# Kernel optimization log

Measured on AMD Instinct MI355X. Metric: run time of the kernel, lower is better.

## Reference

```python
import jax, jax.numpy as jnp
import numpy as np

B, N = 1, 512
CS, CZ, H, CH, PQ, PV = 384, 128, 12, 16, 4, 8
INF, EPS = 1e5, 1e-8
SOFTPLUS_INV_1 = 0.541324854612918


def _init_linear(key, fan_in, fan_out):
    kw, kb = jax.random.split(key)
    std = float(1.0 / np.sqrt(fan_in))
    w = jax.random.normal(kw, (fan_in, fan_out), dtype=jnp.float32) * std
    b = jnp.zeros((fan_out,), dtype=jnp.float32)
    return w, b


def setup_inputs() -> dict:
    key = jax.random.key(0)
    ks = jax.random.split(key, 12)
    s = jax.random.normal(ks[0], (B, N, CS), dtype=jnp.float32)
    z = jax.random.normal(ks[1], (B, N, N, CZ), dtype=jnp.float32) * 0.1
    # proper rotation matrices via QR of random Gaussians
    rot, _ = jnp.linalg.qr(jax.random.normal(ks[2], (B, N, 3, 3), dtype=jnp.float32))
    trans = jax.random.normal(ks[3], (B, N, 3), dtype=jnp.float32) * 10.0
    mask = jnp.ones((B, N), dtype=jnp.float32)
    w_q, b_q = _init_linear(ks[4], CS, H * CH)
    w_kv, b_kv = _init_linear(ks[5], CS, 2 * H * CH)
    w_qp, b_qp = _init_linear(ks[6], CS, H * PQ * 3)
    w_kvp, b_kvp = _init_linear(ks[7], CS, H * (PQ + PV) * 3)
    w_b, b_b = _init_linear(ks[8], CZ, H)
    head_weights = jnp.full((H,), SOFTPLUS_INV_1, dtype=jnp.float32)
    concat_dim = H * (CZ + CH + PV * 4)
    # 'final' init -> zeros
    w_out = jnp.zeros((concat_dim, CS), dtype=jnp.float32)
    b_out = jnp.zeros((CS,), dtype=jnp.float32)
    return dict(s=s, z=z, rot=rot, trans=trans, mask=mask,
                w_q=w_q, b_q=b_q, w_kv=w_kv, b_kv=b_kv,
                w_qp=w_qp, b_qp=b_qp, w_kvp=w_kvp, b_kvp=b_kvp,
                w_b=w_b, b_b=b_b, head_weights=head_weights,
                w_out=w_out, b_out=b_out)


def reference(s, z, rot, trans, mask,
              w_q, b_q, w_kv, b_kv, w_qp, b_qp, w_kvp, b_kvp,
              w_b, b_b, head_weights, w_out, b_out):
    # scalar q/k/v: [B,N,H,CH]
    q = (s @ w_q + b_q).reshape(B, N, H, CH)
    kv = (s @ w_kv + b_kv).reshape(B, N, H, 2 * CH)
    k, v = kv[..., :CH], kv[..., CH:]

    def make_points(w, b, P):
        p = s @ w + b                                   # [B,N,3*H*P] (x|y|z chunks)
        p = jnp.moveaxis(p.reshape(B, N, 3, H * P), -2, -1)  # [B,N,H*P,3]
        p = jnp.einsum('bnij,bnpj->bnpi', rot, p) + trans[:, :, None]  # global frame
        return p.reshape(B, N, H, P, 3)

    q_pts = make_points(w_qp, b_qp, PQ)                 # [B,N,H,PQ,3]
    kv_pts = make_points(w_kvp, b_kvp, PQ + PV)
    k_pts, v_pts = kv_pts[..., :PQ, :], kv_pts[..., PQ:, :]

    # scalar QK attention + pair bias
    a = jnp.einsum('bqhc,bkhc->bhqk', q, k) * float(np.sqrt(1.0 / (3 * CH)))
    b_bias = z @ w_b + b_b                              # [B,N,N,H]
    a = a + float(np.sqrt(1.0 / 3.0)) * jnp.moveaxis(b_bias, -1, -3)

    # squared point-distance attention
    d = q_pts[:, :, None] - k_pts[:, None]              # [B,N,N,H,PQ,3]
    pt_att = jnp.sum(d * d, axis=-1)                    # [B,N,N,H,PQ]
    hw = jax.nn.softplus(head_weights) * float(np.sqrt(1.0 / (3 * (PQ * 9.0 / 2))))
    pt_att = -0.5 * jnp.sum(pt_att * hw[None, None, None, :, None], axis=-1)  # [B,N,N,H]
    a = a + jnp.moveaxis(pt_att, -1, -3)                # [B,H,N,N]

    sq_mask = (mask[:, :, None] * mask[:, None, :] - 1.0) * INF
    a = jax.nn.softmax(a + sq_mask[:, None], axis=-1)   # [B,H,N,N]

    # standard value path
    o = jnp.einsum('bhqk,bkhc->bqhc', a, v).reshape(B, N, H * CH)
    # point value path, rotated back to local frame
    o_pt = jnp.einsum('bhqk,bkhpc->bqhpc', a, v_pts)    # [B,N,H,PV,3]
    o_pt = jnp.einsum('bnji,bnhpj->bnhpi', rot, o_pt - trans[:, :, None, None])
    o_pt_norm = jnp.sqrt(jnp.sum(o_pt ** 2, axis=-1) + EPS).reshape(B, N, H * PV)
    o_pt = o_pt.reshape(B, N, H * PV, 3)
    # pair-weighted path
    o_pair = jnp.einsum('bhqk,bqkc->bqhc', a, z).reshape(B, N, H * CZ)

    o_cat = jnp.concatenate(
        [o, o_pt[..., 0], o_pt[..., 1], o_pt[..., 2], o_pt_norm, o_pair], axis=-1)
    return o_cat @ w_out + b_out
```

## Files before the change

### kernel.cpp

```cpp
#include <hip/hip_runtime.h>
#include <math.h>

#define NRES 512
#define CSD  384
#define CZD  128

#define OFF_Q     0
#define OFF_KT    98304
#define OFF_VC    196608
#define OFF_QP    458752
#define OFF_KPT   532480
#define OFF_A     606208
#define OFF_OCAT  3751936
#define OFF_WCAT  4833280
#define OFF_BCAT  (OFF_WCAT + 442368)
#define OFF_PRAWQ 5276800
#define OFF_PRAWK 5350528
#define OFF_WBT   5571712
#define OFF_PART  OFF_A

__global__ __launch_bounds__(256) void k_wcat(
    const float* __restrict__ w_q, const float* __restrict__ b_q,
    const float* __restrict__ w_kv, const float* __restrict__ b_kv,
    const float* __restrict__ w_qp, const float* __restrict__ b_qp,
    const float* __restrict__ w_kvp, const float* __restrict__ b_kvp,
    const float* __restrict__ w_b,
    float* __restrict__ wcat, float* __restrict__ bcat, float* __restrict__ wbT)
{
    const int idx = blockIdx.x * 256 + threadIdx.x;
    if (idx < 442368) {
        const int k = idx / 1152, c = idx % 1152;
        float v;
        if (c < 192)      v = w_q[k*192 + c];
        else if (c < 576) v = w_kv[k*384 + (c - 192)];
        else if (c < 720) v = w_qp[k*144 + (c - 576)];
        else              v = w_kvp[k*432 + (c - 720)];
        wcat[idx] = v;
    } else if (idx < 443520) {
        const int c = idx - 442368;
        float v;
        if (c < 192)      v = b_q[c];
        else if (c < 576) v = b_kv[c - 192];
        else if (c < 720) v = b_qp[c - 576];
        else              v = b_kvp[c - 720];
        bcat[c] = v;
    } else if (idx < 445056) {
        const int j = idx - 443520;
        const int h = j >> 7, c = j & 127;
        wbT[h*128 + c] = w_b[c*12 + h];
    }
}

__global__ __launch_bounds__(256) void k_proj2(
    const float* __restrict__ s, const float* __restrict__ wcat, const float* __restrict__ bcat,
    float* __restrict__ q, float* __restrict__ kkT, float* __restrict__ vcomb,
    float* __restrict__ praw_q, float* __restrict__ praw_kv)
{
    const int ct = blockIdx.x;
    const int n0 = blockIdx.y * 32;
    const int t = threadIdx.x;

    __shared__ float sT[32][34];
    __shared__ float wt[32][36];

    const int lr = t >> 3, lc4 = t & 7;
    const int tr = t >> 4, tc = t & 15;
    float4 sv4, wv4;

    sv4 = *(const float4*)&s[(n0 + lr) * CSD + lc4 * 4];
    wv4 = *(const float4*)&wcat[lr * 1152 + ct * 32 + lc4 * 4];
    sT[lc4*4+0][lr] = sv4.x; sT[lc4*4+1][lr] = sv4.y; sT[lc4*4+2][lr] = sv4.z; sT[lc4*4+3][lr] = sv4.w;
    *(float4*)&wt[lr][lc4*4] = wv4;
    __syncthreads();

    float a00 = 0.f, a01 = 0.f, a10 = 0.f, a11 = 0.f;

    for (int it = 0; it < 12; ++it) {
        if (it < 11) {
            const int k0 = (it + 1) * 32;
            sv4 = *(const float4*)&s[(n0 + lr) * CSD + k0 + lc4 * 4];
            wv4 = *(const float4*)&wcat[(k0 + lr) * 1152 + ct * 32 + lc4 * 4];
        }
        #pragma unroll
        for (int kx = 0; kx < 32; ++kx) {
            float2 ss = *(const float2*)&sT[kx][tr * 2];
            float2 ww = *(const float2*)&wt[kx][tc * 2];
            a00 += ss.x * ww.x; a01 += ss.x * ww.y;
            a10 += ss.y * ww.x; a11 += ss.y * ww.y;
        }
        __syncthreads();
        if (it < 11) {
            sT[lc4*4+0][lr] = sv4.x; sT[lc4*4+1][lr] = sv4.y; sT[lc4*4+2][lr] = sv4.z; sT[lc4*4+3][lr] = sv4.w;
            *(float4*)&wt[lr][lc4*4] = wv4;
            __syncthreads();
        }
    }

    float accv[2][2] = {{a00, a01}, {a10, a11}};
    #pragma unroll
    for (int i = 0; i < 2; ++i) {
        const int n = n0 + tr * 2 + i;
        #pragma unroll
        for (int j = 0; j < 2; ++j) {
            const int gcol = ct * 32 + tc * 2 + j;
            const float v = accv[i][j] + bcat[gcol];
            if (gcol < 192) {
                q[n*192 + gcol] = v;
            } else if (gcol < 576) {
                int g = gcol - 192, h = g >> 5, cc = g & 31;
                if (cc < 16) kkT[(h*16 + cc)*NRES + n] = v;
                else         vcomb[n*NRES + h*16 + (cc-16)] = v;
            } else if (gcol < 720) {
                praw_q[n*144 + (gcol - 576)] = v;
            } else {
                praw_kv[n*432 + (gcol - 720)] = v;
            }
        }
    }
}

__global__ __launch_bounds__(256) void k_rot(
    const float* __restrict__ praw_q, const float* __restrict__ praw_kv,
    const float* __restrict__ rot, const float* __restrict__ trans,
    float* __restrict__ q_pts, float* __restrict__ kptsT, float* __restrict__ vcomb)
{
    const int idx = blockIdx.x * 256 + threadIdx.x;
    const int n = idx / 192, u = idx % 192;
    const float* R = rot + n*9;
    const float* T = trans + n*3;
    float px, py, pz;
    if (u < 48) {
        px = praw_q[n*144 + u]; py = praw_q[n*144 + 48 + u]; pz = praw_q[n*144 + 96 + u];
    } else {
        int pt = u - 48;
        px = praw_kv[n*432 + pt]; py = praw_kv[n*432 + 144 + pt]; pz = praw_kv[n*432 + 288 + pt];
    }
    float x  = R[0]*px + R[1]*py + R[2]*pz + T[0];
    float y  = R[3]*px + R[4]*py + R[5]*pz + T[1];
    float zc = R[6]*px + R[7]*py + R[8]*pz + T[2];
    if (u < 48) {
        int o = (n*48 + u)*3;
        q_pts[o] = x; q_pts[o+1] = y; q_pts[o+2] = zc;
    } else {
        int pt = u - 48;
        int h = pt / 12, pp = pt % 12;
        if (pp < 4) {
            int dim = (h*4 + pp)*3;
            kptsT[(dim+0)*NRES + n] = x;
            kptsT[(dim+1)*NRES + n] = y;
            kptsT[(dim+2)*NRES + n] = zc;
        } else {
            int u2 = (h*8 + (pp-4))*3;
            vcomb[n*NRES + 192 + u2+0] = x;
            vcomb[n*NRES + 192 + u2+1] = y;
            vcomb[n*NRES + 192 + u2+2] = zc;
        }
    }
}

__global__ __launch_bounds__(256) void k_bias4(
    const float* __restrict__ z, const float* __restrict__ wbT, const float* __restrict__ b_b,
    const float* __restrict__ q, const float* __restrict__ kkT,
    const float* __restrict__ q_pts, const float* __restrict__ kptsT,
    const float* __restrict__ head_weights, const float* __restrict__ mask,
    float* __restrict__ logitsT)
{
    const int k0 = blockIdx.x * 64;
    const int qn = blockIdx.y;
    const int t = threadIdx.x;
    __shared__ float zt[64*128];
    __shared__ float part[4][64][13];
    __shared__ float q_lds[192];
    __shared__ float qp_lds[144];
    __shared__ float hw_lds[12];

    const float4* zp4 = (const float4*)(z + ((size_t)qn*NRES + k0)*CZD);
    float4 zstg[8];
    #pragma unroll
    for (int r = 0; r < 8; ++r) zstg[r] = zp4[t + r*256];
    #pragma unroll
    for (int r = 0; r < 8; ++r) {
        const int idx = t + r*256;
        const int row = idx >> 5, c4 = idx & 31;
        const int sc4 = c4 ^ (row & 7);
        *(float4*)&zt[row*128 + sc4*4] = zstg[r];
    }
    if (t < 192) q_lds[t] = q[qn*192 + t];
    if (t < 144) qp_lds[t] = q_pts[qn*144 + t];
    if (t < 12)  hw_lds[t] = logf(1.f + expf(head_weights[t])) * 0.13608276f;
    __syncthreads();

    {
        const int kgrp = t & 15, cgrp = (t >> 4) & 3, hgrp = t >> 6;
        const int h0 = hgrp * 3;
        const int kx7 = kgrp & 7;
        const float* w0 = wbT + (h0+0)*128 + cgrp*32;
        const float* w1 = wbT + (h0+1)*128 + cgrp*32;
        const float* w2 = wbT + (h0+2)*128 + cgrp*32;
        float acc[4][3];
        #pragma unroll
        for (int kk = 0; kk < 4; ++kk)
            #pragma unroll
            for (int j = 0; j < 3; ++j) acc[kk][j] = 0.f;
        #pragma unroll
        for (int j = 0; j < 8; ++j) {
            const int c4 = cgrp*8 + j;
            const float4 wa  = *(const float4*)&w0[j*4];
            const float4 wbv = *(const float4*)&w1[j*4];
            const float4 wc  = *(const float4*)&w2[j*4];
            const int sc4 = c4 ^ kx7;
            #pragma unroll
            for (int kk = 0; kk < 4; ++kk) {
                const int k = kgrp + 16*kk;
                float4 zv = *(const float4*)&zt[k*128 + sc4*4];
                acc[kk][0] += zv.x*wa.x  + zv.y*wa.y  + zv.z*wa.z  + zv.w*wa.w;
                acc[kk][1] += zv.x*wbv.x + zv.y*wbv.y + zv.z*wbv.z + zv.w*wbv.w;
                acc[kk][2] += zv.x*wc.x  + zv.y*wc.y  + zv.z*wc.z  + zv.w*wc.w;
            }
        }
        #pragma unroll
        for (int kk = 0; kk < 4; ++kk)
            #pragma unroll
            for (int j = 0; j < 3; ++j)
                part[cgrp][kgrp + 16*kk][h0 + j] = acc[kk][j];
    }
    __syncthreads();

    {
        const int k = t & 63;
        const int h0 = (t >> 6) * 3;
        const int kn = k0 + k;
        const float mterm = (mask[qn]*mask[kn] - 1.f) * 100000.f;
        float biasv[3];
        #pragma unroll
        for (int j = 0; j < 3; ++j)
            biasv[j] = b_b[h0+j] + part[0][k][h0+j] + part[1][k][h0+j]
                     + part[2][k][h0+j] + part[3][k][h0+j];
        #pragma unroll
        for (int j = 0; j < 3; ++j) {
            const int h = h0 + j;
            float qk = 0.f;
            const float* kT = kkT + (size_t)(h*16)*NRES + kn;
            #pragma unroll
            for (int c = 0; c < 16; ++c) qk += q_lds[h*16 + c] * kT[(size_t)c*NRES];
            float dsum = 0.f;
            const float* kpT = kptsT + (size_t)(h*12)*NRES + kn;
            #pragma unroll
            for (int d = 0; d < 12; ++d) { float df = qp_lds[h*12 + d] - kpT[(size_t)d*NRES]; dsum += df*df; }
            logitsT[(size_t)h*NRES*NRES + (size_t)qn*NRES + kn] =
                0.14433757f*qk + 0.57735027f*biasv[j] - 0.5f*hw_lds[h]*dsum + mterm;
        }
    }
}

__global__ __launch_bounds__(256) void k_row6(
    const float* __restrict__ z, const float* __restrict__ logitsT,
    const float* __restrict__ vcomb,
    const float* __restrict__ rot, const float* __restrict__ trans,
    float* __restrict__ o_cat)
{
    const int qn = blockIdx.x;
    const int t = threadIdx.x;

    __shared__ float aT[512*20];
    __shared__ float optraw[288];

    for (int i = t; i < 12*NRES; i += 256) {
        const int h = i >> 9, kn = i & 511;
        aT[kn*20 + h] = logitsT[(size_t)h*NRES*NRES + (size_t)qn*NRES + kn];
    }
    __syncthreads();

    {
        const int w = t >> 6, lane = t & 63;
        for (int h = w; h < 12; h += 4) {
            float v[8];
            float m = -1e30f;
            #pragma unroll
            for (int i = 0; i < 8; ++i) {
                v[i] = aT[(lane + i*64)*20 + h];
                m = fmaxf(m, v[i]);
            }
            #pragma unroll
            for (int off = 32; off > 0; off >>= 1) m = fmaxf(m, __shfl_xor(m, off));
            float ss = 0.f;
            #pragma unroll
            for (int i = 0; i < 8; ++i) { v[i] = __expf(v[i] - m); ss += v[i]; }
            #pragma unroll
            for (int off = 32; off > 0; off >>= 1) ss += __shfl_xor(ss, off);
            const float inv = 1.f / ss;
            #pragma unroll
            for (int i = 0; i < 8; ++i) aT[(lane + i*64)*20 + h] = v[i] * inv;
        }
    }
    __syncthreads();

    {
        const int lane = t & 63, w = t >> 6;
        const int c4 = w*8 + (lane & 7);
        const int kg = lane >> 3;
        const float4* zp = (const float4*)(z + (size_t)qn*NRES*CZD) + c4;
        float4 acc4[12];
        #pragma unroll
        for (int h = 0; h < 12; ++h) acc4[h] = make_float4(0.f,0.f,0.f,0.f);

        #pragma unroll 4
        for (int i = 0; i < 64; ++i) {
            const int kn = kg + 8*i;
            float4 zv = zp[(size_t)kn*32];
            float4 a0 = *(const float4*)&aT[kn*20 + 0];
            float4 a1 = *(const float4*)&aT[kn*20 + 4];
            float4 a2 = *(const float4*)&aT[kn*20 + 8];
            float av[12] = {a0.x,a0.y,a0.z,a0.w, a1.x,a1.y,a1.z,a1.w, a2.x,a2.y,a2.z,a2.w};
            #pragma unroll
            for (int h = 0; h < 12; ++h) {
                acc4[h].x += av[h]*zv.x; acc4[h].y += av[h]*zv.y;
                acc4[h].z += av[h]*zv.z; acc4[h].w += av[h]*zv.w;
            }
        }
        #pragma unroll
        for (int h = 0; h < 12; ++h) {
            #pragma unroll
            for (int off = 8; off < 64; off <<= 1) {
                acc4[h].x += __shfl_xor(acc4[h].x, off);
                acc4[h].y += __shfl_xor(acc4[h].y, off);
                acc4[h].z += __shfl_xor(acc4[h].z, off);
                acc4[h].w += __shfl_xor(acc4[h].w, off);
            }
        }
        if (kg == 0) {
            float* ob = o_cat + qn*2112 + 576;
            #pragma unroll
            for (int h = 0; h < 12; ++h)
                *(float4*)&ob[h*128 + c4*4] = acc4[h];
        }
    }

    if (t < 240) {
        const int ch0 = 2*t, ch1 = 2*t + 1;
        const int hA = (ch0 < 192) ? (ch0 >> 4) : (ch0 - 192) / 24;
        const int hB = (ch1 < 192) ? (ch1 >> 4) : (ch1 - 192) / 24;
        float aAcc = 0.f, bAcc = 0.f;
        const float2* vp2 = (const float2*)vcomb + t;
        #pragma unroll 8
        for (int kn = 0; kn < NRES; ++kn) {
            float2 v = vp2[(size_t)kn*256];
            aAcc += aT[kn*20 + hA] * v.x;
            bAcc += aT[kn*20 + hB] * v.y;
        }
        if (ch0 < 192) o_cat[qn*2112 + ch0] = aAcc;
        else           optraw[ch0 - 192] = aAcc;
        if (ch1 < 192) o_cat[qn*2112 + ch1] = bAcc;
        else           optraw[ch1 - 192] = bAcc;
    }
    __syncthreads();

    if (t < 96) {
        const float* R = rot + qn*9;
        const float* T = trans + qn*3;
        float ox = optraw[t*3]   - T[0];
        float oy = optraw[t*3+1] - T[1];
        float oz = optraw[t*3+2] - T[2];
        float x  = R[0]*ox + R[3]*oy + R[6]*oz;
        float y  = R[1]*ox + R[4]*oy + R[7]*oz;
        float zc = R[2]*ox + R[5]*oy + R[8]*oz;
        float* ob = o_cat + qn*2112;
        ob[192 + t] = x;
        ob[288 + t] = y;
        ob[384 + t] = zc;
        ob[480 + t] = sqrtf(x*x + y*y + zc*zc + 1e-8f);
    }
}

__global__ __launch_bounds__(256) void k_out2(
    const float* __restrict__ o_cat, const float* __restrict__ w_out, float* __restrict__ part)
{
    const int ct = blockIdx.x;
    const int n0 = blockIdx.y * 32;
    const int kc = blockIdx.z;
    const int t = threadIdx.x;

    __shared__ float oT[32][34];
    __shared__ float wt[32][36];

    const int lr = t >> 3, lc4 = t & 7;
    const int tr = t >> 4, tc = t & 15;
    const int kbase = kc * 352;
    float4 ov4, wv4;

    ov4 = *(const float4*)&o_cat[(n0 + lr) * 2112 + kbase + lc4 * 4];
    wv4 = *(const float4*)&w_out[(kbase + lr) * 384 + ct * 32 + lc4 * 4];
    oT[lc4*4+0][lr] = ov4.x; oT[lc4*4+1][lr] = ov4.y; oT[lc4*4+2][lr] = ov4.z; oT[lc4*4+3][lr] = ov4.w;
    *(float4*)&wt[lr][lc4*4] = wv4;
    __syncthreads();

    float a00 = 0.f, a01 = 0.f, a10 = 0.f, a11 = 0.f;

    for (int it = 0; it < 11; ++it) {
        if (it < 10) {
            const int k0 = kbase + (it + 1) * 32;
            ov4 = *(const float4*)&o_cat[(n0 + lr) * 2112 + k0 + lc4 * 4];
            wv4 = *(const float4*)&w_out[(k0 + lr) * 384 + ct * 32 + lc4 * 4];
        }
        #pragma unroll
        for (int kx = 0; kx < 32; ++kx) {
            float2 oo = *(const float2*)&oT[kx][tr * 2];
            float2 ww = *(const float2*)&wt[kx][tc * 2];
            a00 += oo.x * ww.x; a01 += oo.x * ww.y;
            a10 += oo.y * ww.x; a11 += oo.y * ww.y;
        }
        __syncthreads();
        if (it < 10) {
            oT[lc4*4+0][lr] = ov4.x; oT[lc4*4+1][lr] = ov4.y; oT[lc4*4+2][lr] = ov4.z; oT[lc4*4+3][lr] = ov4.w;
            *(float4*)&wt[lr][lc4*4] = wv4;
            __syncthreads();
        }
    }

    float* pp = part + (size_t)kc * 196608;
    pp[(n0 + tr*2 + 0)*384 + ct*32 + tc*2 + 0] = a00;
    pp[(n0 + tr*2 + 0)*384 + ct*32 + tc*2 + 1] = a01;
    pp[(n0 + tr*2 + 1)*384 + ct*32 + tc*2 + 0] = a10;
    pp[(n0 + tr*2 + 1)*384 + ct*32 + tc*2 + 1] = a11;
}

__global__ __launch_bounds__(256) void k_red(
    const float* __restrict__ part, const float* __restrict__ b_out, float* __restrict__ out)
{
    const int i = blockIdx.x*256 + threadIdx.x;
    float acc = b_out[i % 384];
    #pragma unroll
    for (int dc = 0; dc < 6; ++dc) acc += part[(size_t)dc*196608 + i];
    out[i] = acc;
}

extern "C" void kernel_launch(void* const* d_in, const int* in_sizes, int n_in,
                              void* d_out, int out_size, void* d_ws, size_t ws_size,
                              hipStream_t stream) {
    (void)in_sizes; (void)n_in; (void)out_size; (void)ws_size;
    const float* s      = (const float*)d_in[0];
    const float* z      = (const float*)d_in[1];
    const float* rot    = (const float*)d_in[2];
    const float* trans  = (const float*)d_in[3];
    const float* mask   = (const float*)d_in[4];
    const float* w_q    = (const float*)d_in[5];
    const float* b_q    = (const float*)d_in[6];
    const float* w_kv   = (const float*)d_in[7];
    const float* b_kv   = (const float*)d_in[8];
    const float* w_qp   = (const float*)d_in[9];
    const float* b_qp   = (const float*)d_in[10];
    const float* w_kvp  = (const float*)d_in[11];
    const float* b_kvp  = (const float*)d_in[12];
    const float* w_b    = (const float*)d_in[13];
    const float* b_b    = (const float*)d_in[14];
    const float* hwts   = (const float*)d_in[15];
    const float* w_out  = (const float*)d_in[16];
    const float* b_out  = (const float*)d_in[17];
    float* out = (float*)d_out;
    float* ws  = (float*)d_ws;

    float* q       = ws + OFF_Q;
    float* kkT     = ws + OFF_KT;
    float* vcomb   = ws + OFF_VC;
    float* qp      = ws + OFF_QP;
    float* kptsT   = ws + OFF_KPT;
    float* logitsT = ws + OFF_A;
    float* ocat    = ws + OFF_OCAT;
    float* wcat    = ws + OFF_WCAT;
    float* bcat    = ws + OFF_BCAT;
    float* wbT     = ws + OFF_WBT;
    float* part    = ws + OFF_PART;
    float* praw_q  = ws + OFF_PRAWQ;
    float* praw_kv = ws + OFF_PRAWK;

    k_wcat<<<dim3(1739), dim3(256), 0, stream>>>(w_q, b_q, w_kv, b_kv, w_qp, b_qp, w_kvp, b_kvp,
        w_b, wcat, bcat, wbT);
    k_proj2<<<dim3(36, 16), dim3(256), 0, stream>>>(s, wcat, bcat, q, kkT, vcomb, praw_q, praw_kv);
    k_rot<<<dim3(384), dim3(256), 0, stream>>>(praw_q, praw_kv, rot, trans, qp, kptsT, vcomb);
    k_bias4<<<dim3(8, NRES), dim3(256), 0, stream>>>(z, wbT, b_b, q, kkT, qp, kptsT,
        hwts, mask, logitsT);
    k_row6<<<dim3(NRES), dim3(256), 0, stream>>>(z, logitsT, vcomb, rot, trans, ocat);
    k_out2<<<dim3(12, 16, 6), dim3(256), 0, stream>>>(ocat, w_out, part);
    k_red<<<dim3(768), dim3(256), 0, stream>>>(part, b_out, out);
}
```

Baseline: 167.2 us.

## Store keys per head-row and split row kernel into softmax, pair, and value kernels

The key and key-point tensors are now stored as contiguous per-(head,residue) rows, so the bias kernel can read them with float4 loads instead of strided column gathers. The fused row kernel is split into three kernels. A standalone softmax kernel normalises the logits in place, one wavefront per row. A pair-weighted z kernel follows, then a separate value and point-value kernel that reads the attention rows straight from global memory. The aim is to cut uncoalesced loads and shrink per-block serial work, at the cost of two extra launches and extra global traffic re-reading the attention matrix.

```diff
diff --git a/kernel.cpp b/kernel.cpp
--- a/kernel.cpp
+++ b/kernel.cpp
@@ -53,7 +53,7 @@
 
 __global__ __launch_bounds__(256) void k_proj2(
     const float* __restrict__ s, const float* __restrict__ wcat, const float* __restrict__ bcat,
-    float* __restrict__ q, float* __restrict__ kkT, float* __restrict__ vcomb,
+    float* __restrict__ q, float* __restrict__ kkP, float* __restrict__ vcomb,
     float* __restrict__ praw_q, float* __restrict__ praw_kv)
 {
     const int ct = blockIdx.x;
@@ -108,7 +108,7 @@
                 q[n*192 + gcol] = v;
             } else if (gcol < 576) {
                 int g = gcol - 192, h = g >> 5, cc = g & 31;
-                if (cc < 16) kkT[(h*16 + cc)*NRES + n] = v;
+                if (cc < 16) kkP[(size_t)(h*NRES + n)*16 + cc] = v;
                 else         vcomb[n*NRES + h*16 + (cc-16)] = v;
             } else if (gcol < 720) {
                 praw_q[n*144 + (gcol - 576)] = v;
@@ -122,7 +122,7 @@
 __global__ __launch_bounds__(256) void k_rot(
     const float* __restrict__ praw_q, const float* __restrict__ praw_kv,
     const float* __restrict__ rot, const float* __restrict__ trans,
-    float* __restrict__ q_pts, float* __restrict__ kptsT, float* __restrict__ vcomb)
+    float* __restrict__ q_pts, float* __restrict__ kptsP, float* __restrict__ vcomb)
 {
     const int idx = blockIdx.x * 256 + threadIdx.x;
     const int n = idx / 192, u = idx % 192;
@@ -145,10 +145,8 @@
         int pt = u - 48;
         int h = pt / 12, pp = pt % 12;
         if (pp < 4) {
-            int dim = (h*4 + pp)*3;
-            kptsT[(dim+0)*NRES + n] = x;
-            kptsT[(dim+1)*NRES + n] = y;
-            kptsT[(dim+2)*NRES + n] = zc;
+            size_t o = (size_t)(h*NRES + n)*12 + pp*3;
+            kptsP[o+0] = x; kptsP[o+1] = y; kptsP[o+2] = zc;
         } else {
             int u2 = (h*8 + (pp-4))*3;
             vcomb[n*NRES + 192 + u2+0] = x;
@@ -160,8 +158,8 @@
 
 __global__ __launch_bounds__(256) void k_bias4(
     const float* __restrict__ z, const float* __restrict__ wbT, const float* __restrict__ b_b,
-    const float* __restrict__ q, const float* __restrict__ kkT,
-    const float* __restrict__ q_pts, const float* __restrict__ kptsT,
+    const float* __restrict__ q, const float* __restrict__ kkP,
+    const float* __restrict__ q_pts, const float* __restrict__ kptsP,
     const float* __restrict__ head_weights, const float* __restrict__ mask,
     float* __restrict__ logitsT)
 {
@@ -239,31 +237,70 @@
         #pragma unroll
         for (int j = 0; j < 3; ++j) {
             const int h = h0 + j;
-            float qk = 0.f;
-            const float* kT = kkT + (size_t)(h*16)*NRES + kn;
-            #pragma unroll
-            for (int c = 0; c < 16; ++c) qk += q_lds[h*16 + c] * kT[(size_t)c*NRES];
-            float dsum = 0.f;
-            const float* kpT = kptsT + (size_t)(h*12)*NRES + kn;
-            #pragma unroll
-            for (int d = 0; d < 12; ++d) { float df = qp_lds[h*12 + d] - kpT[(size_t)d*NRES]; dsum += df*df; }
+            const float* kkrow = kkP + (size_t)(h*NRES + kn)*16;
+            const float* kprow = kptsP + (size_t)(h*NRES + kn)*12;
+            const float4 qv0 = *(const float4*)&q_lds[h*16 + 0];
+            const float4 qv1 = *(const float4*)&q_lds[h*16 + 4];
+            const float4 qv2 = *(const float4*)&q_lds[h*16 + 8];
+            const float4 qv3 = *(const float4*)&q_lds[h*16 + 12];
+            const float4 k0v = *(const float4*)&kkrow[0];
+            const float4 k1v = *(const float4*)&kkrow[4];
+            const float4 k2v = *(const float4*)&kkrow[8];
+            const float4 k3v = *(const float4*)&kkrow[12];
+            float qk = qv0.x*k0v.x + qv0.y*k0v.y + qv0.z*k0v.z + qv0.w*k0v.w
+                     + qv1.x*k1v.x + qv1.y*k1v.y + qv1.z*k1v.z + qv1.w*k1v.w
+                     + qv2.x*k2v.x + qv2.y*k2v.y + qv2.z*k2v.z + qv2.w*k2v.w
+                     + qv3.x*k3v.x + qv3.y*k3v.y + qv3.z*k3v.z + qv3.w*k3v.w;
+            const float4 qp0 = *(const float4*)&qp_lds[h*12 + 0];
+            const float4 qp1 = *(const float4*)&qp_lds[h*12 + 4];
+            const float4 qp2 = *(const float4*)&qp_lds[h*12 + 8];
+            const float4 p0 = *(const float4*)&kprow[0];
+            const float4 p1 = *(const float4*)&kprow[4];
+            const float4 p2 = *(const float4*)&kprow[8];
+            float d0 = qp0.x-p0.x, d1 = qp0.y-p0.y, d2 = qp0.z-p0.z, d3 = qp0.w-p0.w;
+            float d4 = qp1.x-p1.x, d5 = qp1.y-p1.y, d6 = qp1.z-p1.z, d7 = qp1.w-p1.w;
+            float d8 = qp2.x-p2.x, d9 = qp2.y-p2.y, d10 = qp2.z-p2.z, d11 = qp2.w-p2.w;
+            float dsum = d0*d0+d1*d1+d2*d2+d3*d3+d4*d4+d5*d5+d6*d6+d7*d7
+                       + d8*d8+d9*d9+d10*d10+d11*d11;
             logitsT[(size_t)h*NRES*NRES + (size_t)qn*NRES + kn] =
                 0.14433757f*qk + 0.57735027f*biasv[j] - 0.5f*hw_lds[h]*dsum + mterm;
         }
     }
 }
 
-__global__ __launch_bounds__(256) void k_row6(
+__global__ __launch_bounds__(256) void k_sm(float* __restrict__ logitsT)
+{
+    const int lane = threadIdx.x & 63;
+    const int r = blockIdx.x * 4 + (threadIdx.x >> 6);
+    float4* row = (float4*)(logitsT + (size_t)r * NRES);
+
+    float4 v0 = row[lane];
+    float4 v1 = row[lane + 64];
+    float m = fmaxf(fmaxf(fmaxf(v0.x, v0.y), fmaxf(v0.z, v0.w)),
+                    fmaxf(fmaxf(v1.x, v1.y), fmaxf(v1.z, v1.w)));
+    #pragma unroll
+    for (int off = 32; off > 0; off >>= 1) m = fmaxf(m, __shfl_xor(m, off));
+    v0.x = __expf(v0.x - m); v0.y = __expf(v0.y - m);
+    v0.z = __expf(v0.z - m); v0.w = __expf(v0.w - m);
+    v1.x = __expf(v1.x - m); v1.y = __expf(v1.y - m);
+    v1.z = __expf(v1.z - m); v1.w = __expf(v1.w - m);
+    float ss = v0.x + v0.y + v0.z + v0.w + v1.x + v1.y + v1.z + v1.w;
+    #pragma unroll
+    for (int off = 32; off > 0; off >>= 1) ss += __shfl_xor(ss, off);
+    const float inv = 1.f / ss;
+    v0.x *= inv; v0.y *= inv; v0.z *= inv; v0.w *= inv;
+    v1.x *= inv; v1.y *= inv; v1.z *= inv; v1.w *= inv;
+    row[lane] = v0;
+    row[lane + 64] = v1;
+}
+
+__global__ __launch_bounds__(256) void k_pair7(
     const float* __restrict__ z, const float* __restrict__ logitsT,
-    const float* __restrict__ vcomb,
-    const float* __restrict__ rot, const float* __restrict__ trans,
     float* __restrict__ o_cat)
 {
     const int qn = blockIdx.x;
     const int t = threadIdx.x;
-
     __shared__ float aT[512*20];
-    __shared__ float optraw[288];
 
     for (int i = t; i < 12*NRES; i += 256) {
         const int h = i >> 9, kn = i & 511;
@@ -271,82 +308,68 @@
     }
     __syncthreads();
 
-    {
-        const int w = t >> 6, lane = t & 63;
-        for (int h = w; h < 12; h += 4) {
-            float v[8];
-            float m = -1e30f;
-            #pragma unroll
-            for (int i = 0; i < 8; ++i) {
-                v[i] = aT[(lane + i*64)*20 + h];
-                m = fmaxf(m, v[i]);
-            }
-            #pragma unroll
-            for (int off = 32; off > 0; off >>= 1) m = fmaxf(m, __shfl_xor(m, off));
-            float ss = 0.f;
-            #pragma unroll
-            for (int i = 0; i < 8; ++i) { v[i] = __expf(v[i] - m); ss += v[i]; }
-            #pragma unroll
-            for (int off = 32; off > 0; off >>= 1) ss += __shfl_xor(ss, off);
-            const float inv = 1.f / ss;
-            #pragma unroll
-            for (int i = 0; i < 8; ++i) aT[(lane + i*64)*20 + h] = v[i] * inv;
-        }
-    }
-    __syncthreads();
-
-    {
-        const int lane = t & 63, w = t >> 6;
-        const int c4 = w*8 + (lane & 7);
-        const int kg = lane >> 3;
-        const float4* zp = (const float4*)(z + (size_t)qn*NRES*CZD) + c4;
-        float4 acc4[12];
-        #pragma unroll
-        for (int h = 0; h < 12; ++h) acc4[h] = make_float4(0.f,0.f,0.f,0.f);
-
-        #pragma unroll 4
-        for (int i = 0; i < 64; ++i) {
-            const int kn = kg + 8*i;
-            float4 zv = zp[(size_t)kn*32];
-            float4 a0 = *(const float4*)&aT[kn*20 + 0];
-            float4 a1 = *(const float4*)&aT[kn*20 + 4];
-            float4 a2 = *(const float4*)&aT[kn*20 + 8];
-            float av[12] = {a0.x,a0.y,a0.z,a0.w, a1.x,a1.y,a1.z,a1.w, a2.x,a2.y,a2.z,a2.w};
-            #pragma unroll
-            for (int h = 0; h < 12; ++h) {
-                acc4[h].x += av[h]*zv.x; acc4[h].y += av[h]*zv.y;
-                acc4[h].z += av[h]*zv.z; acc4[h].w += av[h]*zv.w;
-            }
-        }
+    const int lane = t & 63, w = t >> 6;
+    const int c4 = w*8 + (lane & 7);
+    const int kg = lane >> 3;
+    const float4* zp = (const float4*)(z + (size_t)qn*NRES*CZD) + c4;
+    float4 acc4[12];
+    #pragma unroll
+    for (int h = 0; h < 12; ++h) acc4[h] = make_float4(0.f,0.f,0.f,0.f);
+
+    #pragma unroll 4
+    for (int i = 0; i < 64; ++i) {
+        const int kn = kg + 8*i;
+        float4 zv = zp[(size_t)kn*32];
+        float4 a0 = *(const float4*)&aT[kn*20 + 0];
+        float4 a1 = *(const float4*)&aT[kn*20 + 4];
+        float4 a2 = *(const float4*)&aT[kn*20 + 8];
+        float av[12] = {a0.x,a0.y,a0.z,a0.w, a1.x,a1.y,a1.z,a1.w, a2.x,a2.y,a2.z,a2.w};
         #pragma unroll
         for (int h = 0; h < 12; ++h) {
-            #pragma unroll
-            for (int off = 8; off < 64; off <<= 1) {
-                acc4[h].x += __shfl_xor(acc4[h].x, off);
-                acc4[h].y += __shfl_xor(acc4[h].y, off);
-                acc4[h].z += __shfl_xor(acc4[h].z, off);
-                acc4[h].w += __shfl_xor(acc4[h].w, off);
-            }
-        }
-        if (kg == 0) {
-            float* ob = o_cat + qn*2112 + 576;
-            #pragma unroll
-            for (int h = 0; h < 12; ++h)
-                *(float4*)&ob[h*128 + c4*4] = acc4[h];
-        }
-    }
+            acc4[h].x += av[h]*zv.x; acc4[h].y += av[h]*zv.y;
+            acc4[h].z += av[h]*zv.z; acc4[h].w += av[h]*zv.w;
+        }
+    }
+    #pragma unroll
+    for (int h = 0; h < 12; ++h) {
+        #pragma unroll
+        for (int off = 8; off < 64; off <<= 1) {
+            acc4[h].x += __shfl_xor(acc4[h].x, off);
+            acc4[h].y += __shfl_xor(acc4[h].y, off);
+            acc4[h].z += __shfl_xor(acc4[h].z, off);
+            acc4[h].w += __shfl_xor(acc4[h].w, off);
+        }
+    }
+    if (kg == 0) {
+        float* ob = o_cat + qn*2112 + 576;
+        #pragma unroll
+        for (int h = 0; h < 12; ++h)
+            *(float4*)&ob[h*128 + c4*4] = acc4[h];
+    }
+}
+
+__global__ __launch_bounds__(256) void k_av2(
+    const float* __restrict__ logitsT, const float* __restrict__ vcomb,
+    const float* __restrict__ rot, const float* __restrict__ trans,
+    float* __restrict__ o_cat)
+{
+    const int qn = blockIdx.x;
+    const int t = threadIdx.x;
+    __shared__ float optraw[288];
 
     if (t < 240) {
         const int ch0 = 2*t, ch1 = 2*t + 1;
         const int hA = (ch0 < 192) ? (ch0 >> 4) : (ch0 - 192) / 24;
         const int hB = (ch1 < 192) ? (ch1 >> 4) : (ch1 - 192) / 24;
+        const float* rowA = logitsT + ((size_t)hA*NRES + qn)*NRES;
+        const float* rowB = logitsT + ((size_t)hB*NRES + qn)*NRES;
+        const float2* vp2 = (const float2*)vcomb + t;
         float aAcc = 0.f, bAcc = 0.f;
-        const float2* vp2 = (const float2*)vcomb + t;
         #pragma unroll 8
         for (int kn = 0; kn < NRES; ++kn) {
             float2 v = vp2[(size_t)kn*256];
-            aAcc += aT[kn*20 + hA] * v.x;
-            bAcc += aT[kn*20 + hB] * v.y;
+            aAcc += rowA[kn] * v.x;
+            bAcc += rowB[kn] * v.y;
         }
         if (ch0 < 192) o_cat[qn*2112 + ch0] = aAcc;
         else           optraw[ch0 - 192] = aAcc;
@@ -460,10 +483,10 @@
     float* ws  = (float*)d_ws;
 
     float* q       = ws + OFF_Q;
-    float* kkT     = ws + OFF_KT;
+    float* kkP     = ws + OFF_KT;
     float* vcomb   = ws + OFF_VC;
     float* qp      = ws + OFF_QP;
-    float* kptsT   = ws + OFF_KPT;
+    float* kptsP   = ws + OFF_KPT;
     float* logitsT = ws + OFF_A;
     float* ocat    = ws + OFF_OCAT;
     float* wcat    = ws + OFF_WCAT;
@@ -475,11 +498,13 @@
 
     k_wcat<<<dim3(1739), dim3(256), 0, stream>>>(w_q, b_q, w_kv, b_kv, w_qp, b_qp, w_kvp, b_kvp,
         w_b, wcat, bcat, wbT);
-    k_proj2<<<dim3(36, 16), dim3(256), 0, stream>>>(s, wcat, bcat, q, kkT, vcomb, praw_q, praw_kv);
-    k_rot<<<dim3(384), dim3(256), 0, stream>>>(praw_q, praw_kv, rot, trans, qp, kptsT, vcomb);
-    k_bias4<<<dim3(8, NRES), dim3(256), 0, stream>>>(z, wbT, b_b, q, kkT, qp, kptsT,
+    k_proj2<<<dim3(36, 16), dim3(256), 0, stream>>>(s, wcat, bcat, q, kkP, vcomb, praw_q, praw_kv);
+    k_rot<<<dim3(384), dim3(256), 0, stream>>>(praw_q, praw_kv, rot, trans, qp, kptsP, vcomb);
+    k_bias4<<<dim3(8, NRES), dim3(256), 0, stream>>>(z, wbT, b_b, q, kkP, qp, kptsP,
         hwts, mask, logitsT);
-    k_row6<<<dim3(NRES), dim3(256), 0, stream>>>(z, logitsT, vcomb, rot, trans, ocat);
+    k_sm<<<dim3(1536), dim3(256), 0, stream>>>(logitsT);
+    k_pair7<<<dim3(NRES), dim3(256), 0, stream>>>(z, logitsT, ocat);
+    k_av2<<<dim3(NRES), dim3(256), 0, stream>>>(logitsT, vcomb, rot, trans, ocat);
     k_out2<<<dim3(12, 16, 6), dim3(256), 0, stream>>>(ocat, w_out, part);
     k_red<<<dim3(768), dim3(256), 0, stream>>>(part, b_out, out);
 }
```

Measured after the change: 189.6 us. 1.13x slower.
